# Kernel tuning notes

Hardware: AMD Instinct MI355X
Metric: run time of the kernel (lower is better)

The kernel has to match this reference:

```python
import jax, jax.numpy as jnp
import numpy as np
from jax import lax

B, S, I, H = 16, 2048, 256, 512


def setup_inputs() -> dict:
    key = jax.random.key(0)
    k = jax.random.split(key, 5)
    s0 = 1.0 / np.sqrt(I + H)
    s1 = 1.0 / np.sqrt(H + H)
    return {
        "x": jax.random.normal(k[0], (B, S, I), dtype=jnp.float32),
        "W0": jax.random.uniform(k[1], (4 * H, I + H), minval=-s0, maxval=s0, dtype=jnp.float32),
        "b0": jax.random.uniform(k[2], (4 * H,), minval=-s0, maxval=s0, dtype=jnp.float32),
        "W1": jax.random.uniform(k[3], (4 * H, H + H), minval=-s1, maxval=s1, dtype=jnp.float32),
        "b1": jax.random.uniform(k[4], (4 * H,), minval=-s1, maxval=s1, dtype=jnp.float32),
    }


def _cell(xt, h, c, W, b):
    # gates: [B, 4H] = cat(xt, h) @ W^T + b
    g = jnp.concatenate([xt, h], axis=1) @ W.T + b
    i_t, f_t, c_tilde, o_t = jnp.split(g, 4, axis=1)
    c_new = jax.nn.sigmoid(f_t) * c + jax.nn.sigmoid(i_t) * jnp.tanh(c_tilde)
    h_new = jax.nn.sigmoid(o_t) * jnp.tanh(c_new)
    return h_new, c_new


def reference(x, W0, b0, W1, b1):
    b, s, _ = x.shape
    hdim = W0.shape[0] // 4
    z = jnp.zeros((b, hdim), dtype=x.dtype)
    init = (z, z, z, z)  # (h0, c0, h1, c1)

    def step(carry, xt):
        h0, c0, h1, c1 = carry
        h0, c0 = _cell(xt, h0, c0, W0, b0)
        h1, c1 = _cell(h0, h1, c1, W1, b1)
        return (h0, c0, h1, c1), h1

    (h0, c0, h1, c1), ys = lax.scan(step, init, jnp.swapaxes(x, 0, 1))
    outputs = jnp.swapaxes(ys, 0, 1)  # [B, S, H] (batch_first=True)
    h = jnp.stack([h0, h1], axis=0)  # [num_layers, B, H]
    c = jnp.stack([c0, c1], axis=0)
    return outputs, (h, c)
```

## Files before the change

### kernel.cpp

```cpp
#include <hip/hip_runtime.h>
#include <hip/hip_bf16.h>


#define BB 16
#define SS 2048
#define II 256
#define HH 512
#define NG0 32
#define NG1 32
#define OUT_H_OFF (BB * SS * HH)
#define OUT_C_OFF (OUT_H_OFF + 2 * BB * HH)

typedef __bf16 bf16x8_t __attribute__((ext_vector_type(8)));
typedef float f32x4_t __attribute__((ext_vector_type(4)));

__device__ __forceinline__ float sigmoidf_(float x) {
    return 1.f / (1.f + __expf(-x));
}
__device__ __forceinline__ float tanhf_(float x) {
    return 1.f - 2.f / (__expf(2.f * x) + 1.f);
}

__device__ __forceinline__ void wait_ge(int* p, int target) {
    while (__hip_atomic_load(p, __ATOMIC_RELAXED, __HIP_MEMORY_SCOPE_AGENT) < target)
        __builtin_amdgcn_s_sleep(1);
}

__device__ __forceinline__ bf16x8_t cvt8(const float* p) {
    f32x4_t a = *reinterpret_cast<const f32x4_t*>(p);
    f32x4_t b = *reinterpret_cast<const f32x4_t*>(p + 4);
    bf16x8_t r;
    r[0] = (__bf16)a[0]; r[1] = (__bf16)a[1];
    r[2] = (__bf16)a[2]; r[3] = (__bf16)a[3];
    r[4] = (__bf16)b[0]; r[5] = (__bf16)b[1];
    r[6] = (__bf16)b[2]; r[7] = (__bf16)b[3];
    return r;
}

__global__ __launch_bounds__(256, 1) void lstm2_persistent(
    const float* __restrict__ x,
    const float* __restrict__ W0,
    const float* __restrict__ b0,
    const float* __restrict__ W1,
    const float* __restrict__ b1,
    float* __restrict__ out,
    int* flag0, int* flag1,
    __bf16* h0buf, __bf16* h1buf)
{
    const int tid = threadIdx.x;
    const int w   = tid >> 6;
    const int l   = tid & 63;
    const int cc  = l & 15;
    const int kg  = l >> 4;
    const int ew_b = tid >> 4;
    const int ew_u = tid & 15;

    __shared__ float gate_s[4][16][17];
    __shared__ float c_s[16][17];

    c_s[ew_u][ew_b] = 0.f;

    if (blockIdx.x < NG0) {
        const int blk   = blockIdx.x;
        const int ubase = blk * 16;
        const int gcol  = w * HH + ubase + cc;
        const float* wrow = W0 + (size_t)gcol * (II + HH);
        bf16x8_t wf[24];
#pragma unroll
        for (int kk = 0; kk < 24; ++kk)
            wf[kk] = cvt8(wrow + kk * 32 + kg * 8);
        const float bias  = b0[gcol];
        const float* xrow = x + (size_t)cc * SS * II;
        __syncthreads();

        for (int t = 0; t < SS; ++t) {
            if (tid == 0) {
                if (t >= 1) wait_ge(flag0 + (t - 1), NG0);
                if (t >= 2) wait_ge(flag1 + (t - 2), NG1);
                __threadfence();
            }
            __syncthreads();

            f32x4_t acc = {0.f, 0.f, 0.f, 0.f};
            const float* xr = xrow + (size_t)t * II;
#pragma unroll
            for (int kk = 0; kk < 8; ++kk) {
                bf16x8_t a = cvt8(xr + kk * 32 + kg * 8);
                acc = __builtin_amdgcn_mfma_f32_16x16x32_bf16(a, wf[kk], acc, 0, 0, 0);
            }
            if (t > 0) {
                const __bf16* hp = h0buf + ((t - 1) & 1) * (BB * HH) + cc * HH + kg * 8;
#pragma unroll
                for (int kk = 8; kk < 24; ++kk) {
                    bf16x8_t a = *reinterpret_cast<const bf16x8_t*>(hp + (kk - 8) * 32);
                    acc = __builtin_amdgcn_mfma_f32_16x16x32_bf16(a, wf[kk], acc, 0, 0, 0);
                }
            }
#pragma unroll
            for (int r = 0; r < 4; ++r)
                gate_s[w][cc][kg * 4 + r] = acc[r] + bias;
            __syncthreads();
            {
                const float gi = gate_s[0][ew_u][ew_b];
                const float gf = gate_s[1][ew_u][ew_b];
                const float gg = gate_s[2][ew_u][ew_b];
                const float go = gate_s[3][ew_u][ew_b];
                const float c  = c_s[ew_u][ew_b];
                const float cn = sigmoidf_(gf) * c + sigmoidf_(gi) * tanhf_(gg);
                const float hn = sigmoidf_(go) * tanhf_(cn);
                c_s[ew_u][ew_b] = cn;
                h0buf[(t & 1) * (BB * HH) + ew_b * HH + ubase + ew_u] = (__bf16)hn;
                if (t == SS - 1) {
                    out[OUT_H_OFF + ew_b * HH + ubase + ew_u] = hn;
                    out[OUT_C_OFF + ew_b * HH + ubase + ew_u] = cn;
                }
            }
            __syncthreads();
            if (tid == 0) {
                __threadfence();
                __hip_atomic_fetch_add(flag0 + t, 1, __ATOMIC_RELEASE,
                                       __HIP_MEMORY_SCOPE_AGENT);
            }
        }
    } else {
        const int blk   = blockIdx.x - NG0;
        const int ubase = blk * 16;
        const int gcol  = w * HH + ubase + cc;
        const float* wrow = W1 + (size_t)gcol * (2 * HH);
        bf16x8_t wf[32];
#pragma unroll
        for (int kk = 0; kk < 32; ++kk)
            wf[kk] = cvt8(wrow + kk * 32 + kg * 8);
        const float bias = b1[gcol];
        __syncthreads();

        for (int t = 0; t < SS; ++t) {
            if (tid == 0) {
                wait_ge(flag0 + t, NG0);
                if (t >= 1) wait_ge(flag1 + (t - 1), NG1);
                __threadfence();
            }
            __syncthreads();

            f32x4_t acc = {0.f, 0.f, 0.f, 0.f};
            const __bf16* h0c = h0buf + (t & 1) * (BB * HH) + cc * HH + kg * 8;
#pragma unroll
            for (int kk = 0; kk < 16; ++kk) {
                bf16x8_t a = *reinterpret_cast<const bf16x8_t*>(h0c + kk * 32);
                acc = __builtin_amdgcn_mfma_f32_16x16x32_bf16(a, wf[kk], acc, 0, 0, 0);
            }
            if (t > 0) {
                const __bf16* h1p = h1buf + ((t - 1) & 1) * (BB * HH) + cc * HH + kg * 8;
#pragma unroll
                for (int kk = 16; kk < 32; ++kk) {
                    bf16x8_t a = *reinterpret_cast<const bf16x8_t*>(h1p + (kk - 16) * 32);
                    acc = __builtin_amdgcn_mfma_f32_16x16x32_bf16(a, wf[kk], acc, 0, 0, 0);
                }
            }
#pragma unroll
            for (int r = 0; r < 4; ++r)
                gate_s[w][cc][kg * 4 + r] = acc[r] + bias;
            __syncthreads();
            {
                const float gi = gate_s[0][ew_u][ew_b];
                const float gf = gate_s[1][ew_u][ew_b];
                const float gg = gate_s[2][ew_u][ew_b];
                const float go = gate_s[3][ew_u][ew_b];
                const float c  = c_s[ew_u][ew_b];
                const float cn = sigmoidf_(gf) * c + sigmoidf_(gi) * tanhf_(gg);
                const float hn = sigmoidf_(go) * tanhf_(cn);
                c_s[ew_u][ew_b] = cn;
                h1buf[(t & 1) * (BB * HH) + ew_b * HH + ubase + ew_u] = (__bf16)hn;
                out[((size_t)ew_b * SS + t) * HH + ubase + ew_u] = hn;
                if (t == SS - 1) {
                    out[OUT_H_OFF + (BB + ew_b) * HH + ubase + ew_u] = hn;
                    out[OUT_C_OFF + (BB + ew_b) * HH + ubase + ew_u] = cn;
                }
            }
            __syncthreads();
            if (tid == 0) {
                __threadfence();
                __hip_atomic_fetch_add(flag1 + t, 1, __ATOMIC_RELEASE,
                                       __HIP_MEMORY_SCOPE_AGENT);
            }
        }
    }
}

extern "C" void kernel_launch(void* const* d_in, const int* in_sizes, int n_in,
                              void* d_out, int out_size, void* d_ws, size_t ws_size,
                              hipStream_t stream) {
    const float* x  = (const float*)d_in[0];
    const float* W0 = (const float*)d_in[1];
    const float* b0 = (const float*)d_in[2];
    const float* W1 = (const float*)d_in[3];
    const float* b1 = (const float*)d_in[4];
    float* out = (float*)d_out;

    char* ws = (char*)d_ws;
    int* flag0 = (int*)ws;
    int* flag1 = (int*)(ws + SS * 4);
    __bf16* h0buf = (__bf16*)(ws + 16384);
    __bf16* h1buf = (__bf16*)(ws + 16384 + 2 * BB * HH * 2);

    hipMemsetAsync(ws, 0, 16384, stream);

    hipLaunchKernelGGL(lstm2_persistent, dim3(NG0 + NG1), dim3(256), 0, stream,
                       x, W0, b0, W1, b1, out, flag0, flag1, h0buf, h1buf);
}
```

Measured before the change: 22.09 ms.

## Replace counter flags with per-block progress flags and overlap input projection with waits

Replaces the per-timestep atomic counters polled by a single thread with per-block progress flags, which a whole wavefront polls in parallel using a vote, and drops the heavy fences in favour of relaxed coherent loads and stores plus vmcnt waits. The x-projection MFMAs are issued before waiting on the previous hidden state. The next timestep's x is prefetched into registers, and layer 1 computes its recurrent h1 part before waiting on layer 0. The MFMA chain is split into four independent accumulators and the cell state is kept in registers. The aim is to shorten the per-step critical path of cross-block synchronisation, at the cost of relying on relaxed memory ordering being correct.

Measured after the change: 21.26 ms. 3.8% less time.

```diff
diff --git a/kernel.cpp b/kernel.cpp
--- a/kernel.cpp
+++ b/kernel.cpp
@@ -8,22 +8,44 @@
 #define HH 512
 #define NG0 32
 #define NG1 32
+#define BHH (BB * HH)
 #define OUT_H_OFF (BB * SS * HH)
 #define OUT_C_OFF (OUT_H_OFF + 2 * BB * HH)
 
 typedef __bf16 bf16x8_t __attribute__((ext_vector_type(8)));
 typedef float f32x4_t __attribute__((ext_vector_type(4)));
 
-__device__ __forceinline__ float sigmoidf_(float x) {
-    return 1.f / (1.f + __expf(-x));
-}
-__device__ __forceinline__ float tanhf_(float x) {
-    return 1.f - 2.f / (__expf(2.f * x) + 1.f);
-}
-
-__device__ __forceinline__ void wait_ge(int* p, int target) {
-    while (__hip_atomic_load(p, __ATOMIC_RELAXED, __HIP_MEMORY_SCOPE_AGENT) < target)
-        __builtin_amdgcn_s_sleep(1);
+union b128u { uint64_t u[2]; bf16x8_t v; };
+
+__device__ __forceinline__ float sigmoidf_(float x) { return 1.f / (1.f + __expf(-x)); }
+__device__ __forceinline__ float tanhf_(float x) { return 1.f - 2.f / (__expf(2.f * x) + 1.f); }
+
+__device__ __forceinline__ uint64_t cload64(const void* p) {
+    return __hip_atomic_load((const uint64_t*)p, __ATOMIC_RELAXED, __HIP_MEMORY_SCOPE_AGENT);
+}
+__device__ __forceinline__ bf16x8_t cload_frag(const __bf16* p) {
+    b128u r;
+    r.u[0] = cload64(p);
+    r.u[1] = cload64(p + 4);
+    return r.v;
+}
+__device__ __forceinline__ void cstore_bf16(__bf16* p, float v) {
+    __bf16 b = (__bf16)v;
+    unsigned short u;
+    __builtin_memcpy(&u, &b, 2);
+    __hip_atomic_store((unsigned short*)p, u, __ATOMIC_RELAXED, __HIP_MEMORY_SCOPE_AGENT);
+}
+
+__device__ __forceinline__ void spin2(const int* f0, int T0, const int* f1, int T1) {
+    const int lidx = threadIdx.x & 63;
+    const int* p = (lidx < 32) ? (f0 + lidx) : (f1 + (lidx - 32));
+    const int tgt = (lidx < 32) ? T0 : T1;
+    while (true) {
+        int v = __hip_atomic_load(p, __ATOMIC_RELAXED, __HIP_MEMORY_SCOPE_AGENT);
+        if (__all(v >= tgt)) break;
+    }
+    __builtin_amdgcn_sched_barrier(0);
+    asm volatile("" ::: "memory");
 }
 
 __device__ __forceinline__ bf16x8_t cvt8(const float* p) {
@@ -36,6 +58,8 @@
     r[6] = (__bf16)b[2]; r[7] = (__bf16)b[3];
     return r;
 }
+
+#define MFMA(A, B, C) __builtin_amdgcn_mfma_f32_16x16x32_bf16((A), (B), (C), 0, 0, 0)
 
 __global__ __launch_bounds__(256, 1) void lstm2_persistent(
     const float* __restrict__ x,
@@ -56,9 +80,7 @@
     const int ew_u = tid & 15;
 
     __shared__ float gate_s[4][16][17];
-    __shared__ float c_s[16][17];
-
-    c_s[ew_u][ew_b] = 0.f;
+    float cstate = 0.f;
 
     if (blockIdx.x < NG0) {
         const int blk   = blockIdx.x;
@@ -71,56 +93,62 @@
             wf[kk] = cvt8(wrow + kk * 32 + kg * 8);
         const float bias  = b0[gcol];
         const float* xrow = x + (size_t)cc * SS * II;
+        bf16x8_t xf[8];
+#pragma unroll
+        for (int kk = 0; kk < 8; ++kk)
+            xf[kk] = cvt8(xrow + kk * 32 + kg * 8);
         __syncthreads();
 
         for (int t = 0; t < SS; ++t) {
-            if (tid == 0) {
-                if (t >= 1) wait_ge(flag0 + (t - 1), NG0);
-                if (t >= 2) wait_ge(flag1 + (t - 2), NG1);
-                __threadfence();
-            }
-            __syncthreads();
-
-            f32x4_t acc = {0.f, 0.f, 0.f, 0.f};
-            const float* xr = xrow + (size_t)t * II;
-#pragma unroll
-            for (int kk = 0; kk < 8; ++kk) {
-                bf16x8_t a = cvt8(xr + kk * 32 + kg * 8);
-                acc = __builtin_amdgcn_mfma_f32_16x16x32_bf16(a, wf[kk], acc, 0, 0, 0);
-            }
+            f32x4_t a0 = {0.f,0.f,0.f,0.f}, a1 = a0, a2 = a0, a3 = a0;
+            a0 = MFMA(xf[0], wf[0], a0); a1 = MFMA(xf[1], wf[1], a1);
+            a2 = MFMA(xf[2], wf[2], a2); a3 = MFMA(xf[3], wf[3], a3);
+            a0 = MFMA(xf[4], wf[4], a0); a1 = MFMA(xf[5], wf[5], a1);
+            a2 = MFMA(xf[6], wf[6], a2); a3 = MFMA(xf[7], wf[7], a3);
+
+            spin2(flag0, t, flag1, t - 1);
+
             if (t > 0) {
-                const __bf16* hp = h0buf + ((t - 1) & 1) * (BB * HH) + cc * HH + kg * 8;
-#pragma unroll
-                for (int kk = 8; kk < 24; ++kk) {
-                    bf16x8_t a = *reinterpret_cast<const bf16x8_t*>(hp + (kk - 8) * 32);
-                    acc = __builtin_amdgcn_mfma_f32_16x16x32_bf16(a, wf[kk], acc, 0, 0, 0);
-                }
-            }
+                const __bf16* hp = h0buf + ((t - 1) & 1) * BHH + cc * HH + kg * 8;
+#pragma unroll
+                for (int kk = 0; kk < 16; kk += 4) {
+                    a0 = MFMA(cload_frag(hp + (kk + 0) * 32), wf[8 + kk + 0], a0);
+                    a1 = MFMA(cload_frag(hp + (kk + 1) * 32), wf[8 + kk + 1], a1);
+                    a2 = MFMA(cload_frag(hp + (kk + 2) * 32), wf[8 + kk + 2], a2);
+                    a3 = MFMA(cload_frag(hp + (kk + 3) * 32), wf[8 + kk + 3], a3);
+                }
+            }
+            f32x4_t acc = (a0 + a1) + (a2 + a3);
 #pragma unroll
             for (int r = 0; r < 4; ++r)
                 gate_s[w][cc][kg * 4 + r] = acc[r] + bias;
+
+            if (t + 1 < SS) {
+                const float* xr = xrow + (size_t)(t + 1) * II;
+#pragma unroll
+                for (int kk = 0; kk < 8; ++kk)
+                    xf[kk] = cvt8(xr + kk * 32 + kg * 8);
+            }
             __syncthreads();
             {
                 const float gi = gate_s[0][ew_u][ew_b];
                 const float gf = gate_s[1][ew_u][ew_b];
                 const float gg = gate_s[2][ew_u][ew_b];
                 const float go = gate_s[3][ew_u][ew_b];
-                const float c  = c_s[ew_u][ew_b];
-                const float cn = sigmoidf_(gf) * c + sigmoidf_(gi) * tanhf_(gg);
+                const float cn = sigmoidf_(gf) * cstate + sigmoidf_(gi) * tanhf_(gg);
                 const float hn = sigmoidf_(go) * tanhf_(cn);
-                c_s[ew_u][ew_b] = cn;
-                h0buf[(t & 1) * (BB * HH) + ew_b * HH + ubase + ew_u] = (__bf16)hn;
+                cstate = cn;
+                cstore_bf16(h0buf + (t & 1) * BHH + ew_b * HH + ubase + ew_u, hn);
                 if (t == SS - 1) {
                     out[OUT_H_OFF + ew_b * HH + ubase + ew_u] = hn;
                     out[OUT_C_OFF + ew_b * HH + ubase + ew_u] = cn;
                 }
             }
-            __syncthreads();
-            if (tid == 0) {
-                __threadfence();
-                __hip_atomic_fetch_add(flag0 + t, 1, __ATOMIC_RELEASE,
-                                       __HIP_MEMORY_SCOPE_AGENT);
-            }
+            asm volatile("s_waitcnt vmcnt(0)" ::: "memory");
+            __syncthreads();
+            if (tid == 0)
+                __hip_atomic_store(flag0 + blk, t + 1, __ATOMIC_RELAXED,
+                                   __HIP_MEMORY_SCOPE_AGENT);
         }
     } else {
         const int blk   = blockIdx.x - NG0;
@@ -135,28 +163,30 @@
         __syncthreads();
 
         for (int t = 0; t < SS; ++t) {
-            if (tid == 0) {
-                wait_ge(flag0 + t, NG0);
-                if (t >= 1) wait_ge(flag1 + (t - 1), NG1);
-                __threadfence();
-            }
-            __syncthreads();
-
-            f32x4_t acc = {0.f, 0.f, 0.f, 0.f};
-            const __bf16* h0c = h0buf + (t & 1) * (BB * HH) + cc * HH + kg * 8;
-#pragma unroll
-            for (int kk = 0; kk < 16; ++kk) {
-                bf16x8_t a = *reinterpret_cast<const bf16x8_t*>(h0c + kk * 32);
-                acc = __builtin_amdgcn_mfma_f32_16x16x32_bf16(a, wf[kk], acc, 0, 0, 0);
-            }
+            f32x4_t a0 = {0.f,0.f,0.f,0.f}, a1 = a0, a2 = a0, a3 = a0;
+            spin2(flag1, t, flag1, t);
             if (t > 0) {
-                const __bf16* h1p = h1buf + ((t - 1) & 1) * (BB * HH) + cc * HH + kg * 8;
-#pragma unroll
-                for (int kk = 16; kk < 32; ++kk) {
-                    bf16x8_t a = *reinterpret_cast<const bf16x8_t*>(h1p + (kk - 16) * 32);
-                    acc = __builtin_amdgcn_mfma_f32_16x16x32_bf16(a, wf[kk], acc, 0, 0, 0);
-                }
-            }
+                const __bf16* h1p = h1buf + ((t - 1) & 1) * BHH + cc * HH + kg * 8;
+#pragma unroll
+                for (int kk = 0; kk < 16; kk += 4) {
+                    a0 = MFMA(cload_frag(h1p + (kk + 0) * 32), wf[16 + kk + 0], a0);
+                    a1 = MFMA(cload_frag(h1p + (kk + 1) * 32), wf[16 + kk + 1], a1);
+                    a2 = MFMA(cload_frag(h1p + (kk + 2) * 32), wf[16 + kk + 2], a2);
+                    a3 = MFMA(cload_frag(h1p + (kk + 3) * 32), wf[16 + kk + 3], a3);
+                }
+            }
+            spin2(flag0, t + 1, flag0, t + 1);
+            {
+                const __bf16* h0c = h0buf + (t & 1) * BHH + cc * HH + kg * 8;
+#pragma unroll
+                for (int kk = 0; kk < 16; kk += 4) {
+                    a0 = MFMA(cload_frag(h0c + (kk + 0) * 32), wf[kk + 0], a0);
+                    a1 = MFMA(cload_frag(h0c + (kk + 1) * 32), wf[kk + 1], a1);
+                    a2 = MFMA(cload_frag(h0c + (kk + 2) * 32), wf[kk + 2], a2);
+                    a3 = MFMA(cload_frag(h0c + (kk + 3) * 32), wf[kk + 3], a3);
+                }
+            }
+            f32x4_t acc = (a0 + a1) + (a2 + a3);
 #pragma unroll
             for (int r = 0; r < 4; ++r)
                 gate_s[w][cc][kg * 4 + r] = acc[r] + bias;
@@ -166,23 +196,21 @@
                 const float gf = gate_s[1][ew_u][ew_b];
                 const float gg = gate_s[2][ew_u][ew_b];
                 const float go = gate_s[3][ew_u][ew_b];
-                const float c  = c_s[ew_u][ew_b];
-                const float cn = sigmoidf_(gf) * c + sigmoidf_(gi) * tanhf_(gg);
+                const float cn = sigmoidf_(gf) * cstate + sigmoidf_(gi) * tanhf_(gg);
                 const float hn = sigmoidf_(go) * tanhf_(cn);
-                c_s[ew_u][ew_b] = cn;
-                h1buf[(t & 1) * (BB * HH) + ew_b * HH + ubase + ew_u] = (__bf16)hn;
+                cstate = cn;
+                cstore_bf16(h1buf + (t & 1) * BHH + ew_b * HH + ubase + ew_u, hn);
                 out[((size_t)ew_b * SS + t) * HH + ubase + ew_u] = hn;
                 if (t == SS - 1) {
                     out[OUT_H_OFF + (BB + ew_b) * HH + ubase + ew_u] = hn;
                     out[OUT_C_OFF + (BB + ew_b) * HH + ubase + ew_u] = cn;
                 }
             }
-            __syncthreads();
-            if (tid == 0) {
-                __threadfence();
-                __hip_atomic_fetch_add(flag1 + t, 1, __ATOMIC_RELEASE,
-                                       __HIP_MEMORY_SCOPE_AGENT);
-            }
+            asm volatile("s_waitcnt vmcnt(0)" ::: "memory");
+            __syncthreads();
+            if (tid == 0)
+                __hip_atomic_store(flag1 + blk, t + 1, __ATOMIC_RELAXED,
+                                   __HIP_MEMORY_SCOPE_AGENT);
         }
     }
 }
@@ -199,11 +227,11 @@
 
     char* ws = (char*)d_ws;
     int* flag0 = (int*)ws;
-    int* flag1 = (int*)(ws + SS * 4);
-    __bf16* h0buf = (__bf16*)(ws + 16384);
-    __bf16* h1buf = (__bf16*)(ws + 16384 + 2 * BB * HH * 2);
-
-    hipMemsetAsync(ws, 0, 16384, stream);
+    int* flag1 = (int*)(ws + 128);
+    __bf16* h0buf = (__bf16*)(ws + 4096);
+    __bf16* h1buf = (__bf16*)(ws + 4096 + 32768);
+
+    hipMemsetAsync(ws, 0, 256, stream);
 
     hipLaunchKernelGGL(lstm2_persistent, dim3(NG0 + NG1), dim3(256), 0, stream,
                        x, W0, b0, W1, b1, out, flag0, flag1, h0buf, h1buf);
```
